# Performance work log

Measured on AMD Instinct MI355X. Metric: run time of the kernel, lower is better.

The kernel has to match this reference:

```python
import jax, jax.numpy as jnp
import numpy as np

B, N, M = 4, 4096, 4096
EPS = 1e-8
LOG_2PI = float(np.log(2.0 * 3.14159))  # module uses 3.14159, not math.pi


def setup_inputs() -> dict:
    key = jax.random.key(0)
    k1, k2, k3 = jax.random.split(key, 3)
    return {
        "pred_xyz": jax.random.normal(k1, (B, N, 3), dtype=jnp.float32),
        "pred_sigma": jax.random.uniform(k2, (B, N, 2), dtype=jnp.float32),
        "target": jax.random.normal(k3, (B, M, 3), dtype=jnp.float32),
    }


def reference(pred_xyz, pred_sigma, target):
    target_xyz = target[:, :, :3]
    # pairwise squared distances: [B, N, M]
    dist_xy = jnp.sum((pred_xyz[:, :, None, :2] - target_xyz[:, None, :, :2]) ** 2, axis=-1)
    dist_z = (pred_xyz[:, :, None, 2] - target_xyz[:, None, :, 2]) ** 2
    sigma_xy = pred_sigma[:, :, 0:1]  # [B, N, 1]
    sigma_z = pred_sigma[:, :, 1:2]   # [B, N, 1]
    log_coef = -jnp.log(sigma_xy + EPS) - 0.5 * jnp.log(sigma_z + EPS)  # [B, N, 1]
    log_probs = (log_coef - 1.5 * LOG_2PI
                 - 0.5 * dist_xy / (sigma_xy + EPS)
                 - 0.5 * dist_z / (sigma_z + EPS))  # [B, N, M]
    nll = -jax.nn.logsumexp(log_probs, axis=1)  # mixture over N predictions -> [B, M]
    return nll.mean()
```

## Files before the change

kernel.cpp:

```cpp
#include <hip/hip_runtime.h>


constexpr int Bc = 4, Nc = 4096, Mc = 4096;
constexpr int NC = 32;
constexpr int NCHUNK = Nc / NC;
constexpr int TM = 8;
constexpr int THREADS = 256;
constexpr int MTILE = THREADS * TM;

#define EPS 1e-8f
constexpr float LOG2E   = 1.4426950408889634f;
constexpr float LN2     = 0.6931471805599453f;
constexpr float LOG_2PI = 1.8378762043478343f;
constexpr float K_CONST = -1.5f * LOG_2PI * LOG2E;

__global__ __launch_bounds__(THREADS, 4) void gmm_partial(
    const float* __restrict__ pred_xyz,
    const float* __restrict__ pred_sigma,
    const float* __restrict__ target,
    float* __restrict__ partials,
    float* __restrict__ out)
{
    __shared__ float4 lds4[NC];
    __shared__ float2 lds2[NC];

    const int nck = blockIdx.x;
    const int mt  = blockIdx.y;
    const int b   = blockIdx.z;
    const int tid = threadIdx.x;
    const int n0  = nck * NC;

    if (nck == 0 && mt == 0 && b == 0 && tid == 0) out[0] = 0.f;

    if (tid < NC) {
        const int n = n0 + tid;
        const float* pp = pred_xyz + ((size_t)b * Nc + n) * 3;
        const float px = pp[0], py = pp[1], pz = pp[2];
        const float* ps = pred_sigma + ((size_t)b * Nc + n) * 2;
        const float sxy = ps[0] + EPS;
        const float sz  = ps[1] + EPS;
        const float A  = -0.5f * LOG2E * __builtin_amdgcn_rcpf(sxy);
        const float C  = -0.5f * LOG2E * __builtin_amdgcn_rcpf(sz);
        const float k2 = -__builtin_amdgcn_logf(sxy)
                         - 0.5f * __builtin_amdgcn_logf(sz)
                         + K_CONST;
        const float K2 = k2 + A * (px * px + py * py) + C * (pz * pz);
        const float Bx = -2.f * A * px;
        const float By = -2.f * A * py;
        const float Cz = -2.f * C * pz;
        lds4[tid] = make_float4(K2, A, C, Bx);
        lds2[tid] = make_float2(By, Cz);
    }
    __syncthreads();

    float tx[TM], ty[TM], tz[TM], txy2[TM], tz2[TM], acc[TM];
    const int m0 = mt * MTILE;
#pragma unroll
    for (int j = 0; j < TM; ++j) {
        const int m = m0 + j * THREADS + tid;
        const float* tp = target + ((size_t)b * Mc + m) * 3;
        tx[j] = tp[0]; ty[j] = tp[1]; tz[j] = tp[2];
        txy2[j] = tx[j] * tx[j] + ty[j] * ty[j];
        tz2[j]  = tz[j] * tz[j];
        acc[j] = 0.f;
    }

#pragma unroll 4
    for (int i = 0; i < NC; ++i) {
        const float4 r0 = lds4[i];
        const float2 r1 = lds2[i];
#pragma unroll
        for (int j = 0; j < TM; ++j) {
            float lp = fmaf(r0.y, txy2[j], r0.x);
            lp = fmaf(r0.z, tz2[j], lp);
            lp = fmaf(r0.w, tx[j], lp);
            lp = fmaf(r1.x, ty[j], lp);
            lp = fmaf(r1.y, tz[j], lp);
            acc[j] += __builtin_amdgcn_exp2f(lp);
        }
    }

    float* dst = partials + ((size_t)b * NCHUNK + nck) * Mc + m0;
#pragma unroll
    for (int j = 0; j < TM; ++j)
        dst[j * THREADS + tid] = acc[j];
}

__global__ __launch_bounds__(256) void gmm_finalize(
    const float* __restrict__ partials, float* __restrict__ out)
{
    const int t = blockIdx.x * 256 + threadIdx.x;
    const int b = t >> 12;
    const int m = t & (Mc - 1);
    const float* src = partials + (size_t)b * NCHUNK * Mc + m;

    float s = 0.f;
#pragma unroll 8
    for (int c = 0; c < NCHUNK; ++c)
        s += src[(size_t)c * Mc];

    float local = __builtin_amdgcn_logf(s);
#pragma unroll
    for (int off = 32; off > 0; off >>= 1)
        local += __shfl_down(local, off, 64);

    __shared__ float w[4];
    const int wave = threadIdx.x >> 6;
    if ((threadIdx.x & 63) == 0) w[wave] = local;
    __syncthreads();
    if (threadIdx.x == 0) {
        const float tot = w[0] + w[1] + w[2] + w[3];
        atomicAdd(out, -LN2 / (float)(Bc * Mc) * tot);
    }
}

extern "C" void kernel_launch(void* const* d_in, const int* in_sizes, int n_in,
                              void* d_out, int out_size, void* d_ws, size_t ws_size,
                              hipStream_t stream) {
    const float* pred_xyz   = (const float*)d_in[0];
    const float* pred_sigma = (const float*)d_in[1];
    const float* target     = (const float*)d_in[2];
    float* out      = (float*)d_out;
    float* partials = (float*)d_ws;

    dim3 grid(NCHUNK, Mc / MTILE, Bc);
    gmm_partial<<<grid, THREADS, 0, stream>>>(pred_xyz, pred_sigma, target,
                                              partials, out);
    gmm_finalize<<<Bc * Mc / 256, 256, 0, stream>>>(partials, out);
}
```

Before: 80.80 us.

## Compute Gaussian log-prob quadratic form with bf16 split-precision MFMA

Recasts the per-pair quadratic form as a rank-6 dot product between precomputed prediction coefficients and target monomials. It evaluates this on MFMA 16x16x32 bf16 instructions, using hi/lo bf16 splitting to recover near-fp32 accuracy. The partition also changes to 8 N-splits with 64-target blocks, which shrinks the partials buffer and the finalize reduction. This moves the FMA work off the vector ALU, but exp2 per element remains and precision may be lower than pure fp32.

```diff
diff --git a/kernel.cpp b/kernel.cpp
--- a/kernel.cpp
+++ b/kernel.cpp
@@ -2,11 +2,12 @@
 
 
 constexpr int Bc = 4, Nc = 4096, Mc = 4096;
-constexpr int NC = 32;
-constexpr int NCHUNK = Nc / NC;
-constexpr int TM = 8;
+constexpr int NSPLIT  = 8;
+constexpr int NCHUNK  = Nc / NSPLIT;
+constexpr int NTILES  = NCHUNK / 16;
 constexpr int THREADS = 256;
-constexpr int MTILE = THREADS * TM;
+constexpr int MBLK    = 64;
+constexpr int REC     = 40;
 
 #define EPS 1e-8f
 constexpr float LOG2E   = 1.4426950408889634f;
@@ -14,76 +15,115 @@
 constexpr float LOG_2PI = 1.8378762043478343f;
 constexpr float K_CONST = -1.5f * LOG_2PI * LOG2E;
 
-__global__ __launch_bounds__(THREADS, 4) void gmm_partial(
+typedef __attribute__((ext_vector_type(8))) short bf16x8;
+typedef __attribute__((ext_vector_type(4))) float f32x4;
+typedef unsigned int   u32;
+typedef unsigned short u16;
+
+static __device__ __forceinline__ u16 f2bf(float x) {
+    u32 u = __float_as_uint(x);
+    return (u16)((u + 0x7fffu + ((u >> 16) & 1u)) >> 16);
+}
+static __device__ __forceinline__ float bf2f(u16 h) {
+    return __uint_as_float((u32)h << 16);
+}
+
+__global__ __launch_bounds__(THREADS) void gmm_partial(
     const float* __restrict__ pred_xyz,
     const float* __restrict__ pred_sigma,
     const float* __restrict__ target,
     float* __restrict__ partials,
     float* __restrict__ out)
 {
-    __shared__ float4 lds4[NC];
-    __shared__ float2 lds2[NC];
+    __shared__ short lds[NCHUNK * REC];
 
-    const int nck = blockIdx.x;
-    const int mt  = blockIdx.y;
-    const int b   = blockIdx.z;
-    const int tid = threadIdx.x;
-    const int n0  = nck * NC;
+    const int mblk = blockIdx.x;
+    const int nck  = blockIdx.y;
+    const int b    = blockIdx.z;
+    const int tid  = threadIdx.x;
 
-    if (nck == 0 && mt == 0 && b == 0 && tid == 0) out[0] = 0.f;
+    if (mblk == 0 && nck == 0 && b == 0 && tid == 0) out[0] = 0.f;
 
-    if (tid < NC) {
-        const int n = n0 + tid;
+    for (int t = tid; t < NCHUNK; t += THREADS) {
+        const int n = nck * NCHUNK + t;
         const float* pp = pred_xyz + ((size_t)b * Nc + n) * 3;
         const float px = pp[0], py = pp[1], pz = pp[2];
         const float* ps = pred_sigma + ((size_t)b * Nc + n) * 2;
         const float sxy = ps[0] + EPS;
         const float sz  = ps[1] + EPS;
-        const float A  = -0.5f * LOG2E * __builtin_amdgcn_rcpf(sxy);
-        const float C  = -0.5f * LOG2E * __builtin_amdgcn_rcpf(sz);
-        const float k2 = -__builtin_amdgcn_logf(sxy)
+        const float A2 = -0.5f * LOG2E * __builtin_amdgcn_rcpf(sxy);
+        const float C2 = -0.5f * LOG2E * __builtin_amdgcn_rcpf(sz);
+        const float K2 = K_CONST - __builtin_amdgcn_logf(sxy)
                          - 0.5f * __builtin_amdgcn_logf(sz)
-                         + K_CONST;
-        const float K2 = k2 + A * (px * px + py * py) + C * (pz * pz);
-        const float Bx = -2.f * A * px;
-        const float By = -2.f * A * py;
-        const float Cz = -2.f * C * pz;
-        lds4[tid] = make_float4(K2, A, C, Bx);
-        lds2[tid] = make_float2(By, Cz);
+                         + A2 * (px * px + py * py) + C2 * (pz * pz);
+        const float Bx = -2.f * A2 * px;
+        const float By = -2.f * A2 * py;
+        const float Cz = -2.f * C2 * pz;
+
+        const u16 h0 = f2bf(K2), h1 = f2bf(A2), h2 = f2bf(C2),
+                  h3 = f2bf(Bx), h4 = f2bf(By), h5 = f2bf(Cz);
+        const u16 l0 = f2bf(K2 - bf2f(h0)), l1 = f2bf(A2 - bf2f(h1)),
+                  l2 = f2bf(C2 - bf2f(h2)), l3 = f2bf(Bx - bf2f(h3)),
+                  l4 = f2bf(By - bf2f(h4)), l5 = f2bf(Cz - bf2f(h5));
+
+        const u32 d0 = (u32)h0 | ((u32)h1 << 16);
+        const u32 d1 = (u32)h2 | ((u32)h3 << 16);
+        const u32 d2 = (u32)h4 | ((u32)h5 << 16);
+        const u32 e0 = (u32)l0 | ((u32)l1 << 16);
+        const u32 e1 = (u32)l2 | ((u32)l3 << 16);
+        const u32 e2 = (u32)l4 | ((u32)l5 << 16);
+        u32* rec = (u32*)&lds[t * REC];
+        rec[0] = d0; rec[1]  = d1; rec[2]  = d2;
+        rec[3] = d0; rec[4]  = d1; rec[5]  = d2;
+        rec[6] = e0; rec[7]  = e1; rec[8]  = e2;
+        rec[9] = 0;  rec[10] = 0;  rec[11] = 0;
+        rec[12] = 0; rec[13] = 0;  rec[14] = 0;  rec[15] = 0;
     }
     __syncthreads();
 
-    float tx[TM], ty[TM], tz[TM], txy2[TM], tz2[TM], acc[TM];
-    const int m0 = mt * MTILE;
-#pragma unroll
-    for (int j = 0; j < TM; ++j) {
-        const int m = m0 + j * THREADS + tid;
-        const float* tp = target + ((size_t)b * Mc + m) * 3;
-        tx[j] = tp[0]; ty[j] = tp[1]; tz[j] = tp[2];
-        txy2[j] = tx[j] * tx[j] + ty[j] * ty[j];
-        tz2[j]  = tz[j] * tz[j];
-        acc[j] = 0.f;
+    const int lane = tid & 63;
+    const int wave = tid >> 6;
+    const int g    = lane >> 4;
+    const int m    = mblk * MBLK + wave * 16 + (lane & 15);
+
+    const float* tp = target + ((size_t)b * Mc + m) * 3;
+    const float tx = tp[0], ty = tp[1], tz = tp[2];
+    const float u1 = tx * tx + ty * ty, u2 = tz * tz;
+
+    const u16 mh0 = f2bf(1.f), mh1 = f2bf(u1), mh2 = f2bf(u2),
+              mh3 = f2bf(tx),  mh4 = f2bf(ty), mh5 = f2bf(tz);
+    const u16 ml0 = 0,
+              ml1 = f2bf(u1 - bf2f(mh1)), ml2 = f2bf(u2 - bf2f(mh2)),
+              ml3 = f2bf(tx - bf2f(mh3)), ml4 = f2bf(ty - bf2f(mh4)),
+              ml5 = f2bf(tz - bf2f(mh5));
+
+    u16 s0, s1, s2, s3, s4, s5, s6, s7;
+    if (g == 0)      { s0=mh0; s1=mh1; s2=mh2; s3=mh3; s4=mh4; s5=mh5; s6=ml0; s7=ml1; }
+    else if (g == 1) { s0=ml2; s1=ml3; s2=ml4; s3=ml5; s4=mh0; s5=mh1; s6=mh2; s7=mh3; }
+    else if (g == 2) { s0=mh4; s1=mh5; s2=0;   s3=0;   s4=0;   s5=0;   s6=0;   s7=0;   }
+    else             { s0=0;   s1=0;   s2=0;   s3=0;   s4=0;   s5=0;   s6=0;   s7=0;   }
+    bf16x8 bfrag;
+    bfrag[0]=(short)s0; bfrag[1]=(short)s1; bfrag[2]=(short)s2; bfrag[3]=(short)s3;
+    bfrag[4]=(short)s4; bfrag[5]=(short)s5; bfrag[6]=(short)s6; bfrag[7]=(short)s7;
+
+    float a0 = 0.f, a1 = 0.f, a2 = 0.f, a3 = 0.f;
+    const short* abase = &lds[(lane & 15) * REC + g * 8];
+    const f32x4 zero4 = {0.f, 0.f, 0.f, 0.f};
+#pragma unroll 4
+    for (int it = 0; it < NTILES; ++it) {
+        bf16x8 afrag = *(const bf16x8*)(abase + it * 16 * REC);
+        f32x4 d = __builtin_amdgcn_mfma_f32_16x16x32_bf16(afrag, bfrag, zero4, 0, 0, 0);
+        a0 += __builtin_amdgcn_exp2f(d[0]);
+        a1 += __builtin_amdgcn_exp2f(d[1]);
+        a2 += __builtin_amdgcn_exp2f(d[2]);
+        a3 += __builtin_amdgcn_exp2f(d[3]);
     }
 
-#pragma unroll 4
-    for (int i = 0; i < NC; ++i) {
-        const float4 r0 = lds4[i];
-        const float2 r1 = lds2[i];
-#pragma unroll
-        for (int j = 0; j < TM; ++j) {
-            float lp = fmaf(r0.y, txy2[j], r0.x);
-            lp = fmaf(r0.z, tz2[j], lp);
-            lp = fmaf(r0.w, tx[j], lp);
-            lp = fmaf(r1.x, ty[j], lp);
-            lp = fmaf(r1.y, tz[j], lp);
-            acc[j] += __builtin_amdgcn_exp2f(lp);
-        }
-    }
-
-    float* dst = partials + ((size_t)b * NCHUNK + nck) * Mc + m0;
-#pragma unroll
-    for (int j = 0; j < TM; ++j)
-        dst[j * THREADS + tid] = acc[j];
+    float s = (a0 + a1) + (a2 + a3);
+    s += __shfl_xor(s, 16, 64);
+    s += __shfl_xor(s, 32, 64);
+    if (g == 0)
+        partials[((size_t)(b * NSPLIT + nck)) * Mc + m] = s;
 }
 
 __global__ __launch_bounds__(256) void gmm_finalize(
@@ -92,14 +132,13 @@
     const int t = blockIdx.x * 256 + threadIdx.x;
     const int b = t >> 12;
     const int m = t & (Mc - 1);
-    const float* src = partials + (size_t)b * NCHUNK * Mc + m;
 
-    float s = 0.f;
-#pragma unroll 8
-    for (int c = 0; c < NCHUNK; ++c)
-        s += src[(size_t)c * Mc];
+    float sum = 0.f;
+#pragma unroll
+    for (int c = 0; c < NSPLIT; ++c)
+        sum += partials[((size_t)(b * NSPLIT + c)) * Mc + m];
 
-    float local = __builtin_amdgcn_logf(s);
+    float local = __builtin_amdgcn_logf(sum);
 #pragma unroll
     for (int off = 32; off > 0; off >>= 1)
         local += __shfl_down(local, off, 64);
@@ -123,7 +162,7 @@
     float* out      = (float*)d_out;
     float* partials = (float*)d_ws;
 
-    dim3 grid(NCHUNK, Mc / MTILE, Bc);
+    dim3 grid(Mc / MBLK, NSPLIT, Bc);
     gmm_partial<<<grid, THREADS, 0, stream>>>(pred_xyz, pred_sigma, target,
                                               partials, out);
     gmm_finalize<<<Bc * Mc / 256, 256, 0, stream>>>(partials, out);
```

Result: faster. 71.21 us (-11.9%).
